# Kernel tuning notes

Hardware: AMD Instinct MI355X
Metric: run time of the kernel (lower is better)

The kernel has to match this reference:

```python
import jax, jax.numpy as jnp
import numpy as np

N_EXPERTS = 8
TOP_K = 2
D_MODEL = 1024
D_FF = 4 * D_MODEL

def setup_inputs() -> dict:
    key = jax.random.key(0)
    ks = jax.random.split(key, 5)
    s_in = 1.0 / np.sqrt(D_MODEL)
    s_ff = 1.0 / np.sqrt(D_FF)
    return {
        "x": jax.random.normal(ks[0], (2, 2048, D_MODEL), dtype=jnp.float32),
        "Wr": jax.random.normal(ks[1], (N_EXPERTS, D_MODEL), dtype=jnp.float32) * s_in,
        "W1": jax.random.normal(ks[2], (N_EXPERTS, D_FF, D_MODEL), dtype=jnp.float32) * s_in,
        "W2": jax.random.normal(ks[3], (N_EXPERTS, D_MODEL, D_FF), dtype=jnp.float32) * s_ff,
        "W3": jax.random.normal(ks[4], (N_EXPERTS, D_FF, D_MODEL), dtype=jnp.float32) * s_in,
    }

def reference(x, Wr, W1, W2, W3):
    B, S, D = x.shape
    T = B * S
    xf = x.reshape(T, D)
    logits = xf @ Wr.T                         # [T, E]
    probs = jax.nn.softmax(logits, axis=-1)
    top_p, top_i = jax.lax.top_k(probs, TOP_K)  # [T, K]
    top_p = top_p / jnp.sum(top_p, axis=-1, keepdims=True)
    # per-token combine weight for each expert: [T, E]
    onehot = jax.nn.one_hot(top_i, N_EXPERTS, dtype=x.dtype)  # [T, K, E]
    cw = jnp.einsum('tke,tk->te', onehot, top_p)
    out = jnp.zeros_like(xf)
    for e in range(N_EXPERTS):  # fixed small structural loop over experts
        h = jax.nn.silu(xf @ W1[e].T) * (xf @ W3[e].T)  # [T, F]
        y = h @ W2[e].T                                 # [T, D]
        out = out + cw[:, e:e+1] * y
    importance = jnp.sum(probs, axis=0)                 # [E]
    load = jnp.sum(jnp.sum(onehot, axis=1), axis=0)     # [E]
    aux_loss = jnp.sum(importance * load) * (N_EXPERTS / (T ** 2 + 1e-06))
    return out.reshape(B, S, D), aux_loss
```

## Files before the change

### kernel.cpp

```cpp
#include <hip/hip_runtime.h>

#define T_TOK 4096
#define DM 1024
#define DF 4096
#define NE 8
#define BM 256
#define RCAP 10240
#define MAXT 40
#define MAXT2 80
#define ACH_B 32768
#define CHUNK_B 8192

typedef _Float16 f16x8 __attribute__((ext_vector_type(8)));
typedef float f32x4 __attribute__((ext_vector_type(4)));

#define MFMA16(a, b, c) __builtin_amdgcn_mfma_f32_16x16x32_f16(a, b, c, 0, 0, 0)
#define RAW_BAR() __builtin_amdgcn_s_barrier()
#define VMCNT(n) asm volatile("s_waitcnt vmcnt(" #n ")" ::: "memory")

__device__ __forceinline__ ushort f2h_bits(float f) {
    _Float16 h = (_Float16)f;
    return __builtin_bit_cast(unsigned short, h);
}

__device__ __forceinline__ unsigned int pk2(float a, float b) {
    return __builtin_bit_cast(unsigned int, __builtin_amdgcn_cvt_pkrtz(a, b));
}

__device__ __forceinline__ uint4 pack8f(float4 a, float4 b) {
    uint4 r;
    r.x = pk2(a.x, a.y); r.y = pk2(a.z, a.w);
    r.z = pk2(b.x, b.y); r.w = pk2(b.z, b.w);
    return r;
}

__device__ __forceinline__ void gll16(const void* g, void* l) {
    __builtin_amdgcn_global_load_lds(
        (const __attribute__((address_space(1))) unsigned int*)g,
        (__attribute__((address_space(3))) unsigned int*)l, 16, 0, 0);
}

__global__ __launch_bounds__(256) void k_init(int* __restrict__ misc,
                                              int* __restrict__ row_tok) {
    int i = blockIdx.x * 256 + threadIdx.x;
    if (i < RCAP) row_tok[i] = -1;
    if (i < 256) misc[i] = 0;
}

__global__ __launch_bounds__(64) void k_router(const float* __restrict__ x,
                                               const float* __restrict__ Wr,
                                               float* __restrict__ probs,
                                               int* __restrict__ topi,
                                               float* __restrict__ topw,
                                               int* __restrict__ cnt) {
    int t = blockIdx.x;
    int lane = threadIdx.x;
    const float* xr = x + (size_t)t * DM;
    float s[NE];
#pragma unroll
    for (int e = 0; e < NE; e++) s[e] = 0.f;
    for (int j = lane; j < DM; j += 64) {
        float xv = xr[j];
#pragma unroll
        for (int e = 0; e < NE; e++) s[e] += xv * Wr[e * DM + j];
    }
#pragma unroll
    for (int off = 32; off > 0; off >>= 1) {
#pragma unroll
        for (int e = 0; e < NE; e++) s[e] += __shfl_xor(s[e], off, 64);
    }
    if (lane == 0) {
        float mx = s[0];
#pragma unroll
        for (int e = 1; e < NE; e++) mx = fmaxf(mx, s[e]);
        float ex[NE], sum = 0.f;
#pragma unroll
        for (int e = 0; e < NE; e++) { ex[e] = expf(s[e] - mx); sum += ex[e]; }
        float inv = 1.f / sum;
        float p[NE];
#pragma unroll
        for (int e = 0; e < NE; e++) { p[e] = ex[e] * inv; probs[t * NE + e] = p[e]; }
        int i0 = 0;
#pragma unroll
        for (int e = 1; e < NE; e++) if (p[e] > p[i0]) i0 = e;
        int i1 = (i0 == 0) ? 1 : 0;
#pragma unroll
        for (int e = 0; e < NE; e++) if (e != i0 && p[e] > p[i1]) i1 = e;
        float w0 = p[i0], w1 = p[i1], winv = 1.f / (w0 + w1);
        topi[2 * t] = i0;     topw[2 * t] = w0 * winv;
        topi[2 * t + 1] = i1; topw[2 * t + 1] = w1 * winv;
        atomicAdd(&cnt[i0], 1);
        atomicAdd(&cnt[i1], 1);
    }
}

__global__ __launch_bounds__(256) void k_scan(const float* __restrict__ probs,
                                              const int* __restrict__ cnt,
                                              int* __restrict__ poff,
                                              int* __restrict__ texp,
                                              int* __restrict__ texp2,
                                              int* __restrict__ ntp,
                                              float* __restrict__ aux_out) {
    __shared__ float red[256 * NE];
    int tid = threadIdx.x;
    float part[NE];
#pragma unroll
    for (int e = 0; e < NE; e++) part[e] = 0.f;
    for (int t = tid; t < T_TOK; t += 256) {
#pragma unroll
        for (int e = 0; e < NE; e++) part[e] += probs[t * NE + e];
    }
#pragma unroll
    for (int e = 0; e < NE; e++) red[tid * NE + e] = part[e];
    __syncthreads();
    for (int s2 = 128; s2 > 0; s2 >>= 1) {
        if (tid < s2) {
#pragma unroll
            for (int e = 0; e < NE; e++) red[tid * NE + e] += red[(tid + s2) * NE + e];
        }
        __syncthreads();
    }
    if (tid == 0) {
        float al = 0.f;
#pragma unroll
        for (int e = 0; e < NE; e++) al += red[e] * (float)cnt[e];
        *aux_out = al * (8.0f / (16777216.0f + 1e-6f));
        int run = 0, tix = 0;
        for (int e = 0; e < NE; e++) {
            poff[e] = run;
            int nt = (cnt[e] + BM - 1) / BM;
            for (int i = 0; i < nt; i++) texp[tix++] = e;
            run += nt * BM;
        }
        ntp[0] = run / BM;
        ntp[1] = run / 128;
        for (int j = 0; j < MAXT2; j++) texp2[j] = (j >> 1) < tix ? texp[j >> 1] : 0;
    }
}

__global__ __launch_bounds__(256) void k_assign(const int* __restrict__ topi,
                                                const float* __restrict__ topw,
                                                const int* __restrict__ poff,
                                                int* __restrict__ fill,
                                                int* __restrict__ row_tok,
                                                int* __restrict__ tok2row) {
    int t = blockIdx.x * 256 + threadIdx.x;
    if (t >= T_TOK) return;
#pragma unroll
    for (int k = 0; k < 2; k++) {
        int e = topi[2 * t + k];
        int pos = atomicAdd(&fill[e], 1);
        int r = poff[e] + pos;
        row_tok[r] = t;
        tok2row[2 * t + k] = r;
    }
}

__global__ __launch_bounds__(256) void k_convert(const float* __restrict__ src,
                                                 ushort* __restrict__ dst,
                                                 int row_len) {
    int nk = row_len >> 6;
    int kt = blockIdx.x, rt = blockIdx.y;
    int tid = threadIdx.x;
    int r = tid >> 2, c0 = (tid & 3) * 16;
    const float* s = src + (size_t)(rt * 64 + r) * row_len + kt * 64 + c0;
    float4 v0 = *(const float4*)(s);
    float4 v1 = *(const float4*)(s + 4);
    float4 v2 = *(const float4*)(s + 8);
    float4 v3 = *(const float4*)(s + 12);
    char* chunk = (char*)dst + ((size_t)rt * nk + kt) * CHUNK_B;
    int sw = (r & 7) << 4;
    *(uint4*)(chunk + r * 128 + ((2 * c0) ^ sw)) = pack8f(v0, v1);
    *(uint4*)(chunk + r * 128 + ((2 * c0 + 16) ^ sw)) = pack8f(v2, v3);
}

__global__ __launch_bounds__(512) void k_gather_t(const float* __restrict__ x,
                                                  const int* __restrict__ row_tok,
                                                  ushort* __restrict__ xg) {
    int kt = blockIdx.x, rt = blockIdx.y;
    int tid = threadIdx.x;
    int r = tid >> 1, c0 = (tid & 1) * 32;
    int tok = row_tok[rt * BM + r];
    char* chunk = (char*)xg + ((size_t)rt * 16 + kt) * ACH_B;
    int sw = (r & 7) << 4;
    if (tok >= 0) {
        const float* s = x + (size_t)tok * DM + kt * 64 + c0;
#pragma unroll
        for (int j = 0; j < 4; j++) {
            float4 va = *(const float4*)(s + j * 8);
            float4 vb = *(const float4*)(s + j * 8 + 4);
            *(uint4*)(chunk + r * 128 + ((c0 * 2 + j * 16) ^ sw)) = pack8f(va, vb);
        }
    } else {
        uint4 z = {0, 0, 0, 0};
#pragma unroll
        for (int j = 0; j < 4; j++)
            *(uint4*)(chunk + r * 128 + ((c0 * 2 + j * 16) ^ sw)) = z;
    }
}

__global__ __launch_bounds__(512, 2) void k_g1(const ushort* __restrict__ xg,
                                               const ushort* __restrict__ W1h,
                                               const ushort* __restrict__ W3h,
                                               const int* __restrict__ texp,
                                               const int* __restrict__ ntp,
                                               ushort* __restrict__ hbuf) {
    __shared__ __align__(16) char lds[131072];
    int b = blockIdx.x;
    int xcd = b & 7, s = b >> 3;
    int rt = (s >> 5) * 8 + ((s >> 2) & 7);
    int ct = xcd * 4 + (s & 3);
    if (rt >= ntp[0]) return;
    int e = texp[rt];
    int tid = threadIdx.x, lane = tid & 63, wv = tid >> 6;
    int wr = wv >> 1, wc = wv & 1;

    const char* Ac  = (const char*)xg + (size_t)rt * 16 * ACH_B;
    const char* B1c = (const char*)W1h + ((size_t)(e * 64 + ct * 2) * 16) * CHUNK_B;
    const char* B3c = (const char*)W3h + ((size_t)(e * 64 + ct * 2) * 16) * CHUNK_B;

    const f32x4 fz = {0.f, 0.f, 0.f, 0.f};
    f32x4 acc1[4][4], acc3[4][4];
#pragma unroll
    for (int m = 0; m < 4; m++)
#pragma unroll
        for (int n = 0; n < 4; n++) { acc1[m][n] = fz; acc3[m][n] = fz; }

    f16x8 af[4], bf[4];
    int kb_base = (lane >> 4) * 16;

#define ST_A(kt_, b_, h_) {                                                        \
        const char* s_ = Ac + (kt_) * ACH_B + (h_) * 16384 + wv * 2048 + lane * 16; \
        char* d_ = lds + (b_) * 65536 + (h_) * 16384 + wv * 2048;                   \
        gll16(s_, d_); gll16(s_ + 1024, d_ + 1024); }
#define ST_B(Bc_, kt_, b_, off_) {                                                          \
        gll16(Bc_ + (kt_) * 8192 + wv * 1024 + lane * 16,                                    \
              lds + (b_) * 65536 + (off_) + wv * 1024);                                      \
        gll16(Bc_ + 131072 + (kt_) * 8192 + wv * 1024 + lane * 16,                           \
              lds + (b_) * 65536 + (off_) + 8192 + wv * 1024); }
#define DS_A(b_, ks_) _Pragma("unroll") for (int m = 0; m < 4; m++) {              \
        int r_ = wr * 64 + m * 16 + (lane & 15);                                   \
        af[m] = *(const f16x8*)(lds + (b_) * 65536 + r_ * 128 +                    \
                                 (((ks_) * 64 + kb_base) ^ ((r_ & 7) << 4))); }
#define DS_B(b_, off_, ks_) _Pragma("unroll") for (int n = 0; n < 4; n++) {        \
        int c_ = wc * 64 + n * 16 + (lane & 15);                                   \
        bf[n] = *(const f16x8*)(lds + (b_) * 65536 + (off_) + c_ * 128 +           \
                                 (((ks_) * 64 + kb_base) ^ ((c_ & 7) << 4))); }
#define MM(accX) _Pragma("unroll") for (int n = 0; n < 4; n++)                     \
        _Pragma("unroll") for (int m = 0; m < 4; m++)                              \
            accX[m][n] = MFMA16(af[m], bf[n], accX[m][n]);

    ST_A(0, 0, 0); ST_A(0, 0, 1); ST_B(B1c, 0, 0, 32768); ST_B(B3c, 0, 0, 49152);
    VMCNT(2);
    RAW_BAR();

    for (int it = 0; it < 8; ++it) {
        int t1 = 2 * it + 1;
        int t2 = 2 * it + 2;
        DS_A(0, 0); DS_B(0, 32768, 0);
        ST_A(t1, 1, 0);
        RAW_BAR();
        __builtin_amdgcn_s_setprio(1); MM(acc1); __builtin_amdgcn_s_setprio(0);
        VMCNT(2);
        RAW_BAR();
        DS_B(0, 49152, 0);
        ST_A(t1, 1, 1);
        RAW_BAR();
        __builtin_amdgcn_s_setprio(1); MM(acc3); __builtin_amdgcn_s_setprio(0);
        RAW_BAR();
        DS_A(0, 1); DS_B(0, 32768, 1);
        ST_B(B1c, t1, 1, 32768);
        RAW_BAR();
        __builtin_amdgcn_s_setprio(1); MM(acc1); __builtin_amdgcn_s_setprio(0);
        RAW_BAR();
        DS_B(0, 49152, 1);
        ST_B(B3c, t1, 1, 49152);
        RAW_BAR();
        __builtin_amdgcn_s_setprio(1); MM(acc3); __builtin_amdgcn_s_setprio(0);
        VMCNT(2);
        RAW_BAR();
        DS_A(1, 0); DS_B(1, 32768, 0);
        if (it < 7) ST_A(t2, 0, 0);
        RAW_BAR();
        __builtin_amdgcn_s_setprio(1); MM(acc1); __builtin_amdgcn_s_setprio(0);
        if (it < 7) { VMCNT(2); } else { VMCNT(0); }
        RAW_BAR();
        DS_B(1, 49152, 0);
        if (it < 7) ST_A(t2, 0, 1);
        RAW_BAR();
        __builtin_amdgcn_s_setprio(1); MM(acc3); __builtin_amdgcn_s_setprio(0);
        RAW_BAR();
        DS_A(1, 1); DS_B(1, 32768, 1);
        if (it < 7) ST_B(B1c, t2, 0, 32768);
        RAW_BAR();
        __builtin_amdgcn_s_setprio(1); MM(acc1); __builtin_amdgcn_s_setprio(0);
        RAW_BAR();
        DS_B(1, 49152, 1);
        if (it < 7) ST_B(B3c, t2, 0, 49152);
        RAW_BAR();
        __builtin_amdgcn_s_setprio(1); MM(acc3); __builtin_amdgcn_s_setprio(0);
        if (it < 7) { VMCNT(2); }
        RAW_BAR();
    }
#undef ST_A
#undef ST_B
#undef DS_A
#undef DS_B
#undef MM

#pragma unroll
    for (int m = 0; m < 4; m++) {
#pragma unroll
        for (int i = 0; i < 4; i++) {
            int rl = wr * 64 + m * 16 + (lane >> 4) * 4 + i;
            int sw = (rl & 7) << 4;
#pragma unroll
            for (int n = 0; n < 4; n++) {
                int fl = wc * 64 + n * 16 + (lane & 15);
                float a1 = acc1[m][n][i], a3 = acc3[m][n][i];
                float h = (a1 / (1.f + expf(-a1))) * a3;
                char* hc = (char*)hbuf + ((size_t)rt * 64 + ct * 2 + (fl >> 6)) * ACH_B;
                *(ushort*)(hc + rl * 128 + ((2 * (fl & 63)) ^ sw)) = f2h_bits(h);
            }
        }
    }
}

__global__ __launch_bounds__(256, 2) void k_g2(const ushort* __restrict__ hbuf,
                                               const ushort* __restrict__ W2h,
                                               const int* __restrict__ texp2,
                                               const int* __restrict__ ntp,
                                               float* __restrict__ ybuf) {
    __shared__ __align__(16) char lds[65536];
    int b = blockIdx.x;
    int xcd = b & 7, s = b >> 3;
    int rt2 = (s >> 3) * 8 + xcd;
    int ct = s & 7;
    if (rt2 >= ntp[1]) return;
    int e = texp2[rt2];
    int tid = threadIdx.x, lane = tid & 63, wv = tid >> 6;
    int wr = wv >> 1, wc = wv & 1;

    const char* Ac = (const char*)hbuf + ((size_t)(rt2 >> 1) * 64) * ACH_B + (rt2 & 1) * 16384;
    const char* Bc = (const char*)W2h + ((size_t)(e * 16 + ct * 2) * 64) * CHUNK_B;

    const f32x4 fz = {0.f, 0.f, 0.f, 0.f};
    f32x4 acc[4][4];
#pragma unroll
    for (int m = 0; m < 4; m++)
#pragma unroll
        for (int n = 0; n < 4; n++) acc[m][n] = fz;

    f16x8 af[4], bf[4];
    int kb_base = (lane >> 4) * 16;

#define ST2_A(kt_, b_) {                                                             \
        const char* s_ = Ac + (size_t)(kt_) * ACH_B + wv * 4096 + lane * 16;         \
        char* d_ = lds + (b_) * 32768 + wv * 4096;                                   \
        gll16(s_, d_); gll16(s_ + 1024, d_ + 1024);                                  \
        gll16(s_ + 2048, d_ + 2048); gll16(s_ + 3072, d_ + 3072); }
#define ST2_B(kt_, b_) {                                                             \
        const char* s0_ = Bc + (size_t)(kt_) * 8192 + wv * 2048 + lane * 16;         \
        char* d0_ = lds + (b_) * 32768 + 16384 + wv * 2048;                          \
        gll16(s0_, d0_); gll16(s0_ + 1024, d0_ + 1024);                              \
        const char* s1_ = Bc + 524288 + (size_t)(kt_) * 8192 + wv * 2048 + lane * 16; \
        char* d1_ = lds + (b_) * 32768 + 24576 + wv * 2048;                          \
        gll16(s1_, d1_); gll16(s1_ + 1024, d1_ + 1024); }
#define DS2_A(b_, ks_) _Pragma("unroll") for (int m = 0; m < 4; m++) {               \
        int r_ = wr * 64 + m * 16 + (lane & 15);                                     \
        af[m] = *(const f16x8*)(lds + (b_) * 32768 + r_ * 128 +                      \
                                 (((ks_) * 64 + kb_base) ^ ((r_ & 7) << 4))); }
#define DS2_B(b_, ks_) _Pragma("unroll") for (int n = 0; n < 4; n++) {               \
        int c_ = wc * 64 + n * 16 + (lane & 15);                                     \
        bf[n] = *(const f16x8*)(lds + (b_) * 32768 + 16384 + c_ * 128 +              \
                                 (((ks_) * 64 + kb_base) ^ ((c_ & 7) << 4))); }
#define MM2() _Pragma("unroll") for (int n = 0; n < 4; n++)                          \
        _Pragma("unroll") for (int m = 0; m < 4; m++)                                \
            acc[m][n] = MFMA16(af[m], bf[n], acc[m][n]);

    ST2_A(0, 0); ST2_B(0, 0);
    VMCNT(0);
    RAW_BAR();

    for (int t = 0; t < 64; ++t) {
        int cur = t & 1;
        DS2_A(cur, 0); DS2_B(cur, 0);
        if (t < 63) { ST2_A(t + 1, cur ^ 1); ST2_B(t + 1, cur ^ 1); }
        RAW_BAR();
        __builtin_amdgcn_s_setprio(1); MM2(); __builtin_amdgcn_s_setprio(0);
        RAW_BAR();
        DS2_A(cur, 1); DS2_B(cur, 1);
        RAW_BAR();
        __builtin_amdgcn_s_setprio(1); MM2(); __builtin_amdgcn_s_setprio(0);
        if (t < 63) { VMCNT(0); }
        RAW_BAR();
    }
#undef ST2_A
#undef ST2_B
#undef DS2_A
#undef DS2_B
#undef MM2

#pragma unroll
    for (int m = 0; m < 4; m++) {
#pragma unroll
        for (int i = 0; i < 4; i++) {
            int rr = rt2 * 128 + wr * 64 + m * 16 + (lane >> 4) * 4 + i;
            float* yrow = ybuf + (size_t)rr * DM + ct * 128 + wc * 64 + (lane & 15);
#pragma unroll
            for (int n = 0; n < 4; n++) yrow[n * 16] = acc[m][n][i];
        }
    }
}

__global__ __launch_bounds__(256) void k_combine(const float* __restrict__ ybuf,
                                                 const int* __restrict__ tok2row,
                                                 const float* __restrict__ topw,
                                                 float* __restrict__ out) {
    int t = blockIdx.x;
    int i = threadIdx.x * 4;
    int r0 = tok2row[2 * t], r1 = tok2row[2 * t + 1];
    float w0 = topw[2 * t], w1 = topw[2 * t + 1];
    float4 a = *(const float4*)(ybuf + (size_t)r0 * DM + i);
    float4 c = *(const float4*)(ybuf + (size_t)r1 * DM + i);
    float4 o;
    o.x = w0 * a.x + w1 * c.x;
    o.y = w0 * a.y + w1 * c.y;
    o.z = w0 * a.z + w1 * c.z;
    o.w = w0 * a.w + w1 * c.w;
    *(float4*)(out + (size_t)t * DM + i) = o;
}

extern "C" void kernel_launch(void* const* d_in, const int* in_sizes, int n_in,
                              void* d_out, int out_size, void* d_ws, size_t ws_size,
                              hipStream_t stream) {
    (void)in_sizes; (void)n_in; (void)out_size; (void)ws_size;
    const float* x  = (const float*)d_in[0];
    const float* Wr = (const float*)d_in[1];
    const float* W1 = (const float*)d_in[2];
    const float* W2 = (const float*)d_in[3];
    const float* W3 = (const float*)d_in[4];
    float* out = (float*)d_out;
    char* ws = (char*)d_ws;

    int* misc  = (int*)ws;
    int* cnt   = misc;
    int* fill  = misc + 8;
    int* poff  = misc + 16;
    int* texp  = misc + 24;
    int* texp2 = misc + 64;
    int* ntp   = misc + 144;
    int*    topi    = (int*)(ws + 1024);
    float*  topw    = (float*)(ws + 33792);
    int*    tok2row = (int*)(ws + 66560);
    float*  probs   = (float*)(ws + 99328);
    int*    row_tok = (int*)(ws + 230400);
    ushort* hbuf    = (ushort*)(ws + 271360);
    ushort* W1h     = (ushort*)(ws + 84157440);
    float*  ybuf    = (float*)(ws + 84157440);
    ushort* W3h     = (ushort*)(ws + 151266304);
    ushort* xg      = (ushort*)(ws + 218375168);
    ushort* W2h     = (ushort*)(ws + 218375168);

    k_init<<<(RCAP + 255) / 256, 256, 0, stream>>>(misc, row_tok);
    k_router<<<T_TOK, 64, 0, stream>>>(x, Wr, probs, topi, topw, cnt);
    k_scan<<<1, 256, 0, stream>>>(probs, cnt, poff, texp, texp2, ntp, out + (size_t)T_TOK * DM);
    k_assign<<<(T_TOK + 255) / 256, 256, 0, stream>>>(topi, topw, poff, fill, row_tok, tok2row);

    k_convert<<<dim3(16, 512), 256, 0, stream>>>(W1, W1h, DM);
    k_convert<<<dim3(16, 512), 256, 0, stream>>>(W3, W3h, DM);
    k_gather_t<<<dim3(16, MAXT), 512, 0, stream>>>(x, row_tok, xg);
    k_g1<<<1280, 512, 0, stream>>>(xg, W1h, W3h, texp, ntp, hbuf);
    k_convert<<<dim3(64, 128), 256, 0, stream>>>(W2, W2h, DF);
    k_g2<<<640, 256, 0, stream>>>(hbuf, W2h, texp2, ntp, ybuf);
    k_combine<<<T_TOK, 256, 0, stream>>>(ybuf, tok2row, topw, out);
}
```

Before: 620.6 us.

## Simplify k_g1 pipeline to whole-tile double buffering with fused W1/W3 MFMAs

```diff
diff --git a/kernel.cpp b/kernel.cpp
--- a/kernel.cpp
+++ b/kernel.cpp
@@ -162,16 +162,19 @@
     int nk = row_len >> 6;
     int kt = blockIdx.x, rt = blockIdx.y;
     int tid = threadIdx.x;
-    int r = tid >> 2, c0 = (tid & 3) * 16;
-    const float* s = src + (size_t)(rt * 64 + r) * row_len + kt * 64 + c0;
-    float4 v0 = *(const float4*)(s);
-    float4 v1 = *(const float4*)(s + 4);
-    float4 v2 = *(const float4*)(s + 8);
-    float4 v3 = *(const float4*)(s + 12);
+    int c0 = (tid & 15) * 4;
     char* chunk = (char*)dst + ((size_t)rt * nk + kt) * CHUNK_B;
-    int sw = (r & 7) << 4;
-    *(uint4*)(chunk + r * 128 + ((2 * c0) ^ sw)) = pack8f(v0, v1);
-    *(uint4*)(chunk + r * 128 + ((2 * c0 + 16) ^ sw)) = pack8f(v2, v3);
+#pragma unroll
+    for (int rr = 0; rr < 4; rr++) {
+        int r = (tid >> 4) + rr * 16;
+        const float* s = src + (size_t)(rt * 64 + r) * row_len + kt * 64 + c0;
+        float4 v = *(const float4*)s;
+        uint2 p;
+        p.x = pk2(v.x, v.y);
+        p.y = pk2(v.z, v.w);
+        int sw = (r & 7) << 4;
+        *(uint2*)(chunk + r * 128 + ((c0 * 2) ^ sw)) = p;
+    }
 }
 
 __global__ __launch_bounds__(512) void k_gather_t(const float* __restrict__ x,
@@ -199,12 +202,12 @@
     }
 }
 
-__global__ __launch_bounds__(512, 2) void k_g1(const ushort* __restrict__ xg,
-                                               const ushort* __restrict__ W1h,
-                                               const ushort* __restrict__ W3h,
-                                               const int* __restrict__ texp,
-                                               const int* __restrict__ ntp,
-                                               ushort* __restrict__ hbuf) {
+__global__ __launch_bounds__(512) void k_g1(const ushort* __restrict__ xg,
+                                            const ushort* __restrict__ W1h,
+                                            const ushort* __restrict__ W3h,
+                                            const int* __restrict__ texp,
+                                            const int* __restrict__ ntp,
+                                            ushort* __restrict__ hbuf) {
     __shared__ __align__(16) char lds[131072];
     int b = blockIdx.x;
     int xcd = b & 7, s = b >> 3;
@@ -226,7 +229,7 @@
 #pragma unroll
         for (int n = 0; n < 4; n++) { acc1[m][n] = fz; acc3[m][n] = fz; }
 
-    f16x8 af[4], bf[4];
+    f16x8 af[4], b1f[4], b3f[4];
     int kb_base = (lane >> 4) * 16;
 
 #define ST_A(kt_, b_, h_) {                                                        \
@@ -242,71 +245,40 @@
         int r_ = wr * 64 + m * 16 + (lane & 15);                                   \
         af[m] = *(const f16x8*)(lds + (b_) * 65536 + r_ * 128 +                    \
                                  (((ks_) * 64 + kb_base) ^ ((r_ & 7) << 4))); }
-#define DS_B(b_, off_, ks_) _Pragma("unroll") for (int n = 0; n < 4; n++) {        \
+#define DS_B(b_, off_, ks_, dst_) _Pragma("unroll") for (int n = 0; n < 4; n++) {  \
         int c_ = wc * 64 + n * 16 + (lane & 15);                                   \
-        bf[n] = *(const f16x8*)(lds + (b_) * 65536 + (off_) + c_ * 128 +           \
+        dst_[n] = *(const f16x8*)(lds + (b_) * 65536 + (off_) + c_ * 128 +         \
                                  (((ks_) * 64 + kb_base) ^ ((c_ & 7) << 4))); }
-#define MM(accX) _Pragma("unroll") for (int n = 0; n < 4; n++)                     \
-        _Pragma("unroll") for (int m = 0; m < 4; m++)                              \
-            accX[m][n] = MFMA16(af[m], bf[n], accX[m][n]);
+#define MM2X() _Pragma("unroll") for (int n = 0; n < 4; n++)                       \
+        _Pragma("unroll") for (int m = 0; m < 4; m++) {                            \
+            acc1[m][n] = MFMA16(af[m], b1f[n], acc1[m][n]);                        \
+            acc3[m][n] = MFMA16(af[m], b3f[n], acc3[m][n]); }
 
     ST_A(0, 0, 0); ST_A(0, 0, 1); ST_B(B1c, 0, 0, 32768); ST_B(B3c, 0, 0, 49152);
-    VMCNT(2);
+    VMCNT(0);
     RAW_BAR();
 
-    for (int it = 0; it < 8; ++it) {
-        int t1 = 2 * it + 1;
-        int t2 = 2 * it + 2;
-        DS_A(0, 0); DS_B(0, 32768, 0);
-        ST_A(t1, 1, 0);
-        RAW_BAR();
-        __builtin_amdgcn_s_setprio(1); MM(acc1); __builtin_amdgcn_s_setprio(0);
-        VMCNT(2);
-        RAW_BAR();
-        DS_B(0, 49152, 0);
-        ST_A(t1, 1, 1);
-        RAW_BAR();
-        __builtin_amdgcn_s_setprio(1); MM(acc3); __builtin_amdgcn_s_setprio(0);
-        RAW_BAR();
-        DS_A(0, 1); DS_B(0, 32768, 1);
-        ST_B(B1c, t1, 1, 32768);
-        RAW_BAR();
-        __builtin_amdgcn_s_setprio(1); MM(acc1); __builtin_amdgcn_s_setprio(0);
-        RAW_BAR();
-        DS_B(0, 49152, 1);
-        ST_B(B3c, t1, 1, 49152);
-        RAW_BAR();
-        __builtin_amdgcn_s_setprio(1); MM(acc3); __builtin_amdgcn_s_setprio(0);
-        VMCNT(2);
-        RAW_BAR();
-        DS_A(1, 0); DS_B(1, 32768, 0);
-        if (it < 7) ST_A(t2, 0, 0);
-        RAW_BAR();
-        __builtin_amdgcn_s_setprio(1); MM(acc1); __builtin_amdgcn_s_setprio(0);
-        if (it < 7) { VMCNT(2); } else { VMCNT(0); }
-        RAW_BAR();
-        DS_B(1, 49152, 0);
-        if (it < 7) ST_A(t2, 0, 1);
-        RAW_BAR();
-        __builtin_amdgcn_s_setprio(1); MM(acc3); __builtin_amdgcn_s_setprio(0);
-        RAW_BAR();
-        DS_A(1, 1); DS_B(1, 32768, 1);
-        if (it < 7) ST_B(B1c, t2, 0, 32768);
-        RAW_BAR();
-        __builtin_amdgcn_s_setprio(1); MM(acc1); __builtin_amdgcn_s_setprio(0);
-        RAW_BAR();
-        DS_B(1, 49152, 1);
-        if (it < 7) ST_B(B3c, t2, 0, 49152);
-        RAW_BAR();
-        __builtin_amdgcn_s_setprio(1); MM(acc3); __builtin_amdgcn_s_setprio(0);
-        if (it < 7) { VMCNT(2); }
+    for (int kt = 0; kt < 16; ++kt) {
+        int cur = kt & 1;
+        DS_A(cur, 0); DS_B(cur, 32768, 0, b1f); DS_B(cur, 49152, 0, b3f);
+        if (kt < 15) {
+            ST_A(kt + 1, cur ^ 1, 0); ST_A(kt + 1, cur ^ 1, 1);
+            ST_B(B1c, kt + 1, cur ^ 1, 32768); ST_B(B3c, kt + 1, cur ^ 1, 49152);
+        }
+        RAW_BAR();
+        __builtin_amdgcn_s_setprio(1); MM2X(); __builtin_amdgcn_s_setprio(0);
+        RAW_BAR();
+        DS_A(cur, 1); DS_B(cur, 32768, 1, b1f); DS_B(cur, 49152, 1, b3f);
+        RAW_BAR();
+        __builtin_amdgcn_s_setprio(1); MM2X(); __builtin_amdgcn_s_setprio(0);
+        if (kt < 15) { VMCNT(0); }
         RAW_BAR();
     }
 #undef ST_A
 #undef ST_B
 #undef DS_A
 #undef DS_B
-#undef MM
+#undef MM2X
 
 #pragma unroll
     for (int m = 0; m < 4; m++) {
```

After: 628.6 us. Within noise of the previous version (+1.3%).
